# Optimization experiments

Hardware: AMD Instinct MI355X
Metric: run time of the kernel (lower is better)

The kernel has to match this reference:

```python
import jax, jax.numpy as jnp
import numpy as np

B, N, E = 16, 512, 131072
FEAT, EMB, H = 3, 512, 3
K1, K2 = 410, 205  # ceil(0.8*512), ceil(0.5*410) per PyG TopKPooling
NEG_SLOPE, EPS = 0.2, 1e-5


def _gat_conv(x, W, att_s, att_d, bias, src, tgt, valid, num_nodes):
    # PyG GATConv (concat=True): per-edge attention with segment softmax over targets.
    Hh, C = att_s.shape
    xp = (x @ W).reshape(-1, Hh, C)                      # [Nn,H,C]
    a_s = jnp.einsum('nhc,hc->nh', xp, att_s)
    a_d = jnp.einsum('nhc,hc->nh', xp, att_d)
    srcc = jnp.where(valid, src, 0)
    tgtc = jnp.where(valid, tgt, 0)
    e = jax.nn.leaky_relu(a_s[srcc] + a_d[tgtc], NEG_SLOPE)  # [Ee,H]
    seg = jnp.where(valid, tgt, num_nodes)               # invalid edges -> dummy segment
    emax = jax.ops.segment_max(e, seg, num_segments=num_nodes + 1)
    emax = jnp.where(jnp.isfinite(emax), emax, 0.0)
    ex = jnp.exp(e - emax[seg]) * valid[:, None].astype(e.dtype)
    den = jax.ops.segment_sum(ex, seg, num_segments=num_nodes + 1)
    alpha = ex / jnp.maximum(den[seg], 1e-16)            # [Ee,H]
    out = jax.ops.segment_sum(alpha[:, :, None] * xp[srcc], seg,
                              num_segments=num_nodes + 1)[:num_nodes]
    return out.reshape(num_nodes, Hh * C) + bias


def _bn(x, g, b):
    # BatchNorm1d, training-mode batch statistics (biased var), eps=1e-5
    m = x.mean(0)
    v = x.var(0)
    return (x - m) * jax.lax.rsqrt(v + EPS) * g + b


def _topk_pool(x, p, nb, n_per, k):
    # PyG TopKPooling: score = tanh(x.w/||w||), keep top-k per graph, scale by score
    score = jnp.tanh((x @ p) / jnp.linalg.norm(p))       # [nb*n_per]
    top_s, top_i = jax.lax.top_k(score.reshape(nb, n_per), k)
    perm = (top_i + jnp.arange(nb)[:, None] * n_per).reshape(-1)
    x_new = x[perm] * top_s.reshape(-1, 1)
    mapping = jnp.full((nb * n_per,), -1, jnp.int32).at[perm].set(
        jnp.arange(nb * k, dtype=jnp.int32))
    return x_new, mapping


def _pool_cat(x, nb, k):
    # [global_max_pool, global_mean_pool] over equal-size graphs
    xr = x.reshape(nb, k, -1)
    return jnp.concatenate([xr.max(1), xr.mean(1)], axis=1)


def _forward(x, W1, as1, ad1, bc1, Wh1, bh1, g1, be1, p1,
             W2, as2, ad2, bc2, Wh2, bh2, g2, be2, p2,
             Wl1, bl1, Wl2, bl2, edge_index):
    Nn = B * N
    src0, tgt0 = edge_index[0], edge_index[1]
    sl = jnp.arange(Nn, dtype=jnp.int32)                 # GATConv add_self_loops=True
    src1 = jnp.concatenate([src0, sl]); tgt1 = jnp.concatenate([tgt0, sl])
    valid1 = jnp.ones(src1.shape, bool)
    h = _gat_conv(x, W1, as1, ad1, bc1, src1, tgt1, valid1, Nn)
    h = jax.nn.relu(h @ Wh1 + bh1)
    h = _bn(h, g1, be1)
    h, mapping = _topk_pool(h, p1, B, N, K1)
    x1 = _pool_cat(h, B, K1)                             # [B, 2*EMB]
    # relabel edges to pooled node ids; drop edges with removed endpoints via mask
    s2 = mapping[src0]; t2 = mapping[tgt0]
    v2 = (s2 >= 0) & (t2 >= 0)
    sl2 = jnp.arange(B * K1, dtype=jnp.int32)
    src2 = jnp.concatenate([s2, sl2]); tgt2 = jnp.concatenate([t2, sl2])
    valid2 = jnp.concatenate([v2, jnp.ones(sl2.shape, bool)])
    h = _gat_conv(h, W2, as2, ad2, bc2, src2, tgt2, valid2, B * K1)
    h = jax.nn.relu(h @ Wh2 + bh2)
    h = _bn(h, g2, be2)
    h, _ = _topk_pool(h, p2, B, K1, K2)
    x2 = _pool_cat(h, B, K2)
    xg = x1 + x2
    xg = jax.nn.relu(xg @ Wl1 + bl1)                     # dropout p=0.5 disabled (eval)
    return xg @ Wl2 + bl2                                # [B, 256]


def setup_inputs() -> dict:
    key = jax.random.key(0)
    ks = jax.random.split(key, 16)
    x = jax.random.normal(ks[0], (B * N, FEAT), jnp.float32)
    goff = jnp.repeat(jnp.arange(B, dtype=jnp.int32), E // B) * N
    src = jax.random.randint(ks[1], (E,), 0, N, jnp.int32) + goff
    tgt = jax.random.randint(ks[2], (E,), 0, N, jnp.int32) + goff
    edge_index = jnp.stack([src, tgt])
    s = 0.05
    p = {
        'W1': jax.random.normal(ks[3], (FEAT, H * EMB)) * s,
        'as1': jax.random.normal(ks[4], (H, EMB)) * s,
        'ad1': jax.random.normal(ks[5], (H, EMB)) * s,
        'bc1': jnp.zeros((H * EMB,)),
        'Wh1': jax.random.normal(ks[6], (H * EMB, EMB)) * s,
        'bh1': jnp.zeros((EMB,)),
        'g1': jnp.ones((EMB,)), 'be1': jnp.zeros((EMB,)),
        'p1': jax.random.normal(ks[7], (EMB,)) * s,
        'W2': jax.random.normal(ks[8], (EMB, H * EMB)) * s,
        'as2': jax.random.normal(ks[9], (H, EMB)) * s,
        'ad2': jax.random.normal(ks[10], (H, EMB)) * s,
        'bc2': jnp.zeros((H * EMB,)),
        'Wh2': jax.random.normal(ks[11], (H * EMB, EMB)) * s,
        'bh2': jnp.zeros((EMB,)),
        'g2': jnp.ones((EMB,)), 'be2': jnp.zeros((EMB,)),
        'p2': jax.random.normal(ks[12], (EMB,)) * s,
        'Wl1': jax.random.normal(ks[13], (2 * EMB, 512)) * s,
        'bl1': jnp.zeros((512,)),
        'Wl2': jax.random.normal(ks[14], (512, 256)) * s,
        'bl2': jnp.zeros((256,)),
    }
    return {'x': x, 'edge_index': edge_index, **p}


def reference(x, edge_index, W1, as1, ad1, bc1, Wh1, bh1, g1, be1, p1,
              W2, as2, ad2, bc2, Wh2, bh2, g2, be2, p2, Wl1, bl1, Wl2, bl2):
    return _forward(x, W1, as1, ad1, bc1, Wh1, bh1, g1, be1, p1,
                    W2, as2, ad2, bc2, Wh2, bh2, g2, be2, p2,
                    Wl1, bl1, Wl2, bl2, edge_index)
```

## Files before the change

### kernel.cpp

```cpp
#include <hip/hip_runtime.h>
#include <hip/hip_bf16.h>
#include <math.h>

#define E_EDGES 131072
#define NN1 8192
#define NN2 6560
#define NG 16
#define NP1 512
#define KP1 410
#define KP2 205
#define F1 1536
#define EMB 512
#define MAXDEG 256

typedef __hip_bfloat16 bf16;
typedef __attribute__((ext_vector_type(8))) short short8;
typedef __attribute__((ext_vector_type(4))) float f32x4;
typedef __attribute__((ext_vector_type(4))) unsigned short us4;

__device__ inline float wred64(float v){
  #pragma unroll
  for (int o = 32; o; o >>= 1) v += __shfl_down(v, o);
  return v;
}
__device__ inline float b2f_raw(unsigned short u){
  return __uint_as_float((unsigned)u << 16);
}
union BFU { bf16 b; unsigned short u; };
__device__ inline unsigned short f2u(float v){ BFU x; x.b = __float2bfloat16(v); return x.u; }

__device__ __forceinline__ void gld16(const void* g, void* l){
  __builtin_amdgcn_global_load_lds(
      (const __attribute__((address_space(1))) void*)g,
      (__attribute__((address_space(3))) void*)l, 16, 0, 0);
}

__device__ inline void split_store(float v, bf16* __restrict__ ph, bf16* __restrict__ pl){
  bf16 hi = __float2bfloat16(v);
  *ph = hi;
  *pl = __float2bfloat16(v - __bfloat162float(hi));
}

__device__ inline void bn_from_acc(const float* __restrict__ bnacc, int c, float fM,
                                   float& mean, float& inv){
  mean = bnacc[c] / fM;
  float var = fmaxf(bnacc[512+c]/fM - mean*mean, 0.f);
  inv = 1.f / sqrtf(var + 1e-5f);
}

__global__ __launch_bounds__(256) void k_pre(
    const float* __restrict__ W1, const float* __restrict__ as1, const float* __restrict__ ad1,
    const float* __restrict__ Wh1, const float* __restrict__ bc1, const float* __restrict__ bh1,
    const float* __restrict__ W2, const float* __restrict__ as2, const float* __restrict__ ad2,
    const float* __restrict__ Wh2, const float* __restrict__ bc2, const float* __restrict__ bh2,
    const int* __restrict__ src0, const int* __restrict__ tgt0, const float* __restrict__ x,
    float* __restrict__ M1p, float* __restrict__ cvp,
    float* __restrict__ was2, float* __restrict__ wad2,
    float* __restrict__ Zb, int* __restrict__ cnt2, int* __restrict__ map,
    bf16* __restrict__ Th, bf16* __restrict__ Tl,
    float* __restrict__ denp, float* __restrict__ nump){
  int b = blockIdx.x, t = threadIdx.x;
  if (b < 24){
    int h = b / 8, rem = b % 8, jh = rem >> 2, kc = rem & 3;
    int j = jh*256 + t, c0 = kc*128;
    __shared__ float w1s[3][128];
    for (int i = t; i < 384; i += 256)
      w1s[i>>7][i&127] = W1[(i>>7)*1536 + h*512 + c0 + (i&127)];
    __syncthreads();
    const float* whc = Wh1 + (size_t)(h*512 + c0)*512 + j;
    float a0=0.f, a1=0.f, a2=0.f;
    #pragma unroll 8
    for (int c = 0; c < 128; c++){
      float v = whc[(size_t)c*512];
      a0 += w1s[0][c]*v; a1 += w1s[1][c]*v; a2 += w1s[2][c]*v;
    }
    float* dst = M1p + (size_t)kc*4608;
    dst[(h*3+0)*512 + j] = a0;
    dst[(h*3+1)*512 + j] = a1;
    dst[(h*3+2)*512 + j] = a2;
  } else if (b < 56){
    int b2 = b - 24;
    int which = b2 >> 4, rem = b2 & 15, jh = rem >> 3, kc = rem & 7;
    const float* bc = which ? bc2 : bc1;
    const float* Wh = which ? Wh2 : Wh1;
    const float* bh = which ? bh2 : bh1;
    int j = jh*256 + t, i0 = kc*192;
    float acc = (kc == 0) ? bh[j] : 0.f;
    #pragma unroll 8
    for (int i = 0; i < 192; i++)
      acc += bc[i0+i] * Wh[(size_t)(i0+i)*512 + j];
    cvp[(size_t)(which*8 + kc)*512 + j] = acc;
  } else if (b < 152){
    int b3 = b - 56;
    int y = b3 >> 4, et = b3 & 15;
    int kind = y / 3, h = y % 3;
    int w = t >> 6, lane = t & 63;
    const float* att = kind ? ad2 : as2;
    float a[8];
    #pragma unroll
    for (int u = 0; u < 8; u++) a[u] = att[h*512 + lane*8 + u];
    for (int r = w; r < 32; r += 4){
      int e = et*32 + r;
      const float4* row = (const float4*)(W2 + (size_t)e*1536 + h*512) + lane*2;
      float4 v0 = row[0], v1 = row[1];
      float d = v0.x*a[0]+v0.y*a[1]+v0.z*a[2]+v0.w*a[3]
              + v1.x*a[4]+v1.y*a[5]+v1.z*a[6]+v1.w*a[7];
      d = wred64(d);
      if (lane == 0) (kind ? wad2 : was2)[h*512 + e] = d;
    }
  } else if (b < 218){
    int i = (b - 152)*256 + t;
    if (i < 2048){ Zb[i] = 0.f; }
    else if (i < 2048 + NN2){ cnt2[i - 2048] = 1; }
    else if (i < 2048 + NN2 + NN1){ map[i - 2048 - NN2] = -1; }
  } else if (b < 474){
    __shared__ float sww[18];
    __shared__ float lden[1536];
    __shared__ float lnum[4608];
    int wv_ = t >> 6, lane = t & 63;
    for (int combo = wv_*5; combo < wv_*5+5 && combo < 18; combo++){
      int kind = combo/9, rr = combo%9, h = rr/3, f = rr%3;
      const float* att = kind ? ad1 : as1;
      float s = 0.f;
      #pragma unroll
      for (int c = lane; c < 512; c += 64) s += W1[f*1536 + h*512 + c] * att[h*512 + c];
      s = wred64(s);
      if (lane == 0) sww[combo] = s;
    }
    for (int i = t; i < 1536; i += 256) lden[i] = 0.f;
    for (int i = t; i < 4608; i += 256) lnum[i] = 0.f;
    __syncthreads();
    int eb = b - 218;
    int g = eb >> 4, ch = eb & 15;
    int base = g*8192;
    int it0 = ch*544;
    for (int k = t; k < 544; k += 256){
      int it = it0 + k;
      int s, tl;
      if (it < 8192){ s = src0[base+it]; tl = tgt0[base+it] & 511; }
      else { tl = it - 8192; s = g*512 + tl; }
      float xs0 = x[s*3], xs1 = x[s*3+1], xs2 = x[s*3+2];
      int tg = g*512 + tl;
      float xt0 = x[tg*3], xt1 = x[tg*3+1], xt2 = x[tg*3+2];
      #pragma unroll
      for (int h = 0; h < 3; h++){
        float v = xs0*sww[h*3]+xs1*sww[h*3+1]+xs2*sww[h*3+2]
                + xt0*sww[9+h*3]+xt1*sww[9+h*3+1]+xt2*sww[9+h*3+2];
        v = v > 0.f ? v : 0.2f*v;
        float pe = expf(v);
        atomicAdd(&lden[tl*3 + h], pe);
        atomicAdd(&lnum[tl*9 + h*3 + 0], pe * xs0);
        atomicAdd(&lnum[tl*9 + h*3 + 1], pe * xs1);
        atomicAdd(&lnum[tl*9 + h*3 + 2], pe * xs2);
      }
    }
    __syncthreads();
    for (int i = t; i < 4608; i += 256) nump[(size_t)eb*4608 + i] = lnum[i];
    for (int i = t; i < 1536; i += 256) denp[(size_t)eb*1536 + i] = lden[i];
  } else {
    int bb = b - 474;
    int z = bb % 3; int rr = bb / 3; int by = rr >> 3, bx = rr & 7;
    const float* A = W2 + (size_t)z*512;
    const float* B = Wh2 + (size_t)z*512*512;
    __shared__ __align__(16) short sAh[4096], sAl[4096], sBh[4096], sBl[4096];
    int w = t >> 6, lane = t & 63;
    int l16 = lane & 15, q = lane >> 4;
    int bm = by*64, bn = bx*64;
    int am  = t >> 2, akw = (t & 3)*16;
    int bnl = t & 63, bkq = (t >> 6)*16;
    f32x4 acc[4];
    #pragma unroll
    for (int nf = 0; nf < 4; nf++) acc[nf] = (f32x4){0.f,0.f,0.f,0.f};
    float va[16], vb[16];
    #define GS_LOAD(K0) do { \
      _Pragma("unroll") for (int u = 0; u < 4; u++){ \
        float4 v4 = *(const float4*)(A + (size_t)(bm+am)*1536 + (K0) + akw + u*4); \
        va[u*4]=v4.x; va[u*4+1]=v4.y; va[u*4+2]=v4.z; va[u*4+3]=v4.w; } \
      _Pragma("unroll") for (int u = 0; u < 16; u++) \
        vb[u] = B[(size_t)((K0) + bkq + u)*512 + bn + bnl]; \
    } while(0)
    GS_LOAD(0);
    for (int it = 0; it < 8; it++){
      #pragma unroll
      for (int hh = 0; hh < 2; hh++){
        short8 ah_, al_, bh_, bl_;
        #pragma unroll
        for (int jj = 0; jj < 8; jj++){
          float v = va[hh*8+jj];
          unsigned short hu = f2u(v);
          ah_[jj] = (short)hu; al_[jj] = (short)f2u(v - b2f_raw(hu));
          v = vb[hh*8+jj];
          hu = f2u(v);
          bh_[jj] = (short)hu; bl_[jj] = (short)f2u(v - b2f_raw(hu));
        }
        int aoff = am*64  + ((((akw>>3) + hh) ^ (am  & 7)) << 3);
        *(short8*)(sAh + aoff) = ah_;
        *(short8*)(sAl + aoff) = al_;
        int boff = bnl*64 + ((((bkq>>3) + hh) ^ (bnl & 7)) << 3);
        *(short8*)(sBh + boff) = bh_;
        *(short8*)(sBl + boff) = bl_;
      }
      __syncthreads();
      if (it < 7) GS_LOAD((it+1)*64);
      #pragma unroll
      for (int ks = 0; ks < 2; ks++){
        int gc = ks*4 + q;
        int ar = w*16 + l16;
        int ao = ar*64 + ((gc ^ (ar & 7)) << 3);
        short8 afh = *(const short8*)(sAh + ao);
        short8 afl = *(const short8*)(sAl + ao);
        #pragma unroll
        for (int nf = 0; nf < 4; nf++){
          int br = nf*16 + l16;
          int bo = br*64 + ((gc ^ (br & 7)) << 3);
          short8 bfh = *(const short8*)(sBh + bo);
          short8 bfl = *(const short8*)(sBl + bo);
          acc[nf] = __builtin_amdgcn_mfma_f32_16x16x32_bf16(afh, bfh, acc[nf], 0, 0, 0);
          acc[nf] = __builtin_amdgcn_mfma_f32_16x16x32_bf16(afh, bfl, acc[nf], 0, 0, 0);
          acc[nf] = __builtin_amdgcn_mfma_f32_16x16x32_bf16(afl, bfh, acc[nf], 0, 0, 0);
        }
      }
      __syncthreads();
    }
    #undef GS_LOAD
    int m0 = bm + w*16 + q*4;
    #pragma unroll
    for (int nf = 0; nf < 4; nf++){
      int n = bn + nf*16 + l16;
      size_t base = (size_t)n*1536 + (size_t)z*512 + m0;
      #pragma unroll
      for (int e = 0; e < 4; e++)
        split_store(acc[nf][e], &Th[base+e], &Tl[base+e]);
    }
  }
}

__global__ __launch_bounds__(256) void k_h1(
    const float* __restrict__ nump, const float* __restrict__ denp,
    const float* __restrict__ M1p, const float* __restrict__ cvp1, bf16* __restrict__ hout,
    float* __restrict__ bnacc1){
  __shared__ float sM[9*512];
  __shared__ float sC[512];
  __shared__ float sA[32*9];
  int t = threadIdx.x; int n0 = blockIdx.x*32;
  for (int i = t; i < 9*512; i += 256)
    sM[i] = M1p[i] + M1p[4608 + i] + M1p[2*4608 + i] + M1p[3*4608 + i];
  for (int i = t; i < 512; i += 256){
    float s = 0.f;
    #pragma unroll
    for (int kc = 0; kc < 8; kc++) s += cvp1[kc*512 + i];
    sC[i] = s;
  }
  for (int i = t; i < 288; i += 256){
    int node = i / 9, q = i % 9, hh = q / 3;
    int gn = n0 + node;
    int g = gn >> 9, nl = gn & 511;
    float ns = 0.f, ds = 0.f;
    #pragma unroll 4
    for (int ch = 0; ch < 16; ch++){
      ns += nump[(size_t)(g*16 + ch)*4608 + nl*9 + q];
      ds += denp[(size_t)(g*16 + ch)*1536 + nl*3 + hh];
    }
    sA[i] = ns / fmaxf(ds, 1e-16f);
  }
  __syncthreads();
  float c0v = sC[t], c1v = sC[t+256];
  float ls0=0.f, lq0=0.f, ls1=0.f, lq1=0.f;
  #pragma unroll 4
  for (int i = 0; i < 32; i++){
    float a0 = c0v, a1 = c1v;
    #pragma unroll
    for (int q = 0; q < 9; q++){
      float av = sA[i*9+q];
      a0 += av * sM[q*512 + t];
      a1 += av * sM[q*512 + t + 256];
    }
    a0 = fmaxf(a0, 0.f); a1 = fmaxf(a1, 0.f);
    hout[(size_t)(n0+i)*512 + t]       = __float2bfloat16(a0);
    hout[(size_t)(n0+i)*512 + t + 256] = __float2bfloat16(a1);
    ls0 += a0; lq0 += a0*a0; ls1 += a1; lq1 += a1*a1;
  }
  atomicAdd(&bnacc1[t],           ls0);
  atomicAdd(&bnacc1[t+256],       ls1);
  atomicAdd(&bnacc1[512 + t],     lq0);
  atomicAdd(&bnacc1[512 + t+256], lq1);
}

__global__ __launch_bounds__(512) void k_scoresort(
    const bf16* __restrict__ h, const float* __restrict__ bnacc, int M,
    const float* __restrict__ g_, const float* __restrict__ be, const float* __restrict__ p,
    int n_per, int K, int* __restrict__ map,
    int* __restrict__ topi, float* __restrict__ tops, float* __restrict__ cat){
  int g = blockIdx.x, t = threadIdx.x;
  __shared__ float w[512];
  __shared__ float redb[8], redp[8];
  __shared__ float sk[512];
  __shared__ int si[512];
  float fM = (float)M;
  float mean, inv; bn_from_acc(bnacc, t, fM, mean, inv);
  float gc = g_[t], pc = p[t], bec = be[t];
  float ig = inv * gc;
  w[t] = ig * pc;
  float bt = (bec - mean * ig) * pc;
  float b_ = wred64(bt);
  float pp = wred64(pc * pc);
  int lane = t & 63, wv = t >> 6;
  if (lane == 0){ redb[wv] = b_; redp[wv] = pp; }
  __syncthreads();
  float B0 = 0.f, pn2 = 0.f;
  #pragma unroll
  for (int u = 0; u < 8; u++){ B0 += redb[u]; pn2 += redp[u]; }
  float pn = sqrtf(pn2);
  float score = -INFINITY; int idx = 0x7fffffff;
  if (t < n_per){
    const unsigned short* hr = (const unsigned short*)h + (size_t)(g*n_per + t)*EMB;
    float dot = 0.f;
    #pragma unroll 4
    for (int c = 0; c < 512; c += 8){
      us4 v0 = *(const us4*)(hr + c);
      us4 v1 = *(const us4*)(hr + c + 4);
      dot += b2f_raw(v0.x)*w[c]   + b2f_raw(v0.y)*w[c+1]
           + b2f_raw(v0.z)*w[c+2] + b2f_raw(v0.w)*w[c+3]
           + b2f_raw(v1.x)*w[c+4] + b2f_raw(v1.y)*w[c+5]
           + b2f_raw(v1.z)*w[c+6] + b2f_raw(v1.w)*w[c+7];
    }
    score = tanhf((dot + B0) / pn);
    idx = t;
  }
  sk[t] = score; si[t] = idx;
  __syncthreads();
  for (int k = 2; k <= 512; k <<= 1){
    for (int j = k >> 1; j > 0; j >>= 1){
      int l = t ^ j;
      if (l > t){
        float ki = sk[t], kl = sk[l]; int ii = si[t], il = si[l];
        bool before_l = (kl > ki) || (kl == ki && il < ii);
        bool up = ((t & k) == 0);
        if (up == before_l){ sk[t]=kl; sk[l]=ki; si[t]=il; si[l]=ii; }
      }
      __syncthreads();
    }
  }
  if (cat == nullptr){
    if (t < K){
      if (map) map[g*n_per + si[t]] = g*K + t;
      topi[g*K + t] = si[t];
      tops[g*K + t] = sk[t];
    }
  } else {
    const unsigned short* hp = (const unsigned short*)h;
    float mx = -INFINITY, sm = 0.f;
    for (int r = 0; r < K; r++){
      float v = (b2f_raw(hp[(size_t)(g*n_per + si[r])*EMB + t]) - mean) * ig + bec;
      v *= sk[r];
      mx = fmaxf(mx, v); sm += v;
    }
    cat[g*1024 + t] = mx;
    cat[g*1024 + 512 + t] = sm / (float)K;
  }
}

__global__ __launch_bounds__(256) void k_gather_c2(
    const bf16* __restrict__ h, const float* __restrict__ bnacc, int M,
    const float* __restrict__ gm, const float* __restrict__ be,
    const int* __restrict__ topi, const float* __restrict__ tops,
    bf16* __restrict__ xn, int n_per, int K,
    const float* __restrict__ was2, const float* __restrict__ wad2,
    float* __restrict__ aso, float* __restrict__ ado,
    const int* __restrict__ src0, const int* __restrict__ tgt0,
    const int* __restrict__ map, int* __restrict__ cnt2, int nblk_g){
  int row = blockIdx.x, t = threadIdx.x;
  if (row >= nblk_g){
    int i = (row - nblk_g)*256 + t;
    if (i < E_EDGES){
      int s = map[src0[i]], tg = map[tgt0[i]];
      if (s >= 0 && tg >= 0) atomicAdd(&cnt2[tg], 1);
    }
    return;
  }
  int gr = row / K, i = row - gr*K;
  int sidx = topi[gr*K + i];
  float s = tops[gr*K + i];
  const bf16* src = h + ((size_t)(gr*n_per + sidx))*EMB;
  bf16* dst = xn + (size_t)row*EMB;
  int c0 = t, c1 = t + 256;
  float fM = (float)M;
  float mean0, inv0, mean1, inv1;
  bn_from_acc(bnacc, c0, fM, mean0, inv0);
  bn_from_acc(bnacc, c1, fM, mean1, inv1);
  float v0 = ((__bfloat162float(src[c0]) - mean0) * inv0 * gm[c0] + be[c0]) * s;
  float v1 = ((__bfloat162float(src[c1]) - mean1) * inv1 * gm[c1] + be[c1]) * s;
  dst[c0] = __float2bfloat16(v0);
  dst[c1] = __float2bfloat16(v1);
  {
    float a[6];
    #pragma unroll
    for (int hh = 0; hh < 3; hh++){
      a[hh]   = v0*was2[hh*512 + c0] + v1*was2[hh*512 + c1];
      a[3+hh] = v0*wad2[hh*512 + c0] + v1*wad2[hh*512 + c1];
    }
    __shared__ float red[6][4];
    int lane = t & 63, wv = t >> 6;
    #pragma unroll
    for (int q = 0; q < 6; q++){ float v = wred64(a[q]); if (lane==0) red[q][wv]=v; }
    __syncthreads();
    if (t < 6){
      float sm = red[t][0]+red[t][1]+red[t][2]+red[t][3];
      if (t < 3) aso[row*3+t] = sm; else ado[row*3+(t-3)] = sm;
    }
  }
}

__device__ inline void scan_body(const int* __restrict__ counts, int* __restrict__ off,
                                 int* __restrict__ cur, int n, int* __restrict__ sh){
  int t = threadIdx.x;
  int chunk = (n + 1023) >> 10;
  int b = t * chunk; int e = b + chunk; if (e > n) e = n;
  int s = 0;
  for (int i = b; i < e; i++) s += counts[i];
  sh[t] = s; __syncthreads();
  for (int o = 1; o < 1024; o <<= 1){
    int v = (t >= o) ? sh[t-o] : 0;
    __syncthreads();
    sh[t] += v;
    __syncthreads();
  }
  int run = (t > 0) ? sh[t-1] : 0;
  for (int i = b; i < e; i++){ int c = counts[i]; off[i] = run; cur[i] = run; run += c; }
  if (t == 1023) off[n] = sh[1023];
}
__global__ void k_fill2(const int* __restrict__ src0, const int* __restrict__ tgt0,
                        const int* __restrict__ map, int* __restrict__ cur,
                        int* __restrict__ esrc, int E, int nn){
  int i = blockIdx.x*blockDim.x + threadIdx.x;
  if (i >= E + nn) return;
  int s, tg;
  if (i < E){
    s = map[src0[i]]; tg = map[tgt0[i]];
    if (s < 0 || tg < 0) return;
  } else { s = i - E; tg = s; }
  int pos = atomicAdd(&cur[tg], 1);
  esrc[pos] = s;
}

__global__ __launch_bounds__(1024) void k_poolA_scan(const bf16* __restrict__ xn,
    float* __restrict__ cat, int K,
    const int* __restrict__ cnt2, int* __restrict__ off2, int* __restrict__ cur2){
  __shared__ int shi[1024];
  __shared__ float smax[8][128];
  __shared__ float ssum[8][128];
  int b = blockIdx.x, t = threadIdx.x;
  if (b == 64){ scan_body(cnt2, off2, cur2, NN2, shi); return; }
  int g = b >> 2, cb = b & 3;
  int c = t & 127, rg = t >> 7;
  int col = cb*128 + c;
  const unsigned short* p = (const unsigned short*)xn + (size_t)g*K*EMB + col;
  float mx = -INFINITY, sm = 0.f;
  for (int r = rg; r < K; r += 8){
    float v = b2f_raw(p[(size_t)r*EMB]);
    mx = fmaxf(mx, v); sm += v;
  }
  smax[rg][c] = mx; ssum[rg][c] = sm;
  __syncthreads();
  if (rg == 0){
    #pragma unroll
    for (int u = 1; u < 8; u++){ mx = fmaxf(mx, smax[u][c]); sm += ssum[u][c]; }
    cat[g*1024 + col] = mx;
    cat[g*1024 + 512 + col] = sm / (float)K;
  }
}

__global__ __launch_bounds__(256) void k_agg2(
    const bf16* __restrict__ xn, const float* __restrict__ aso, const float* __restrict__ ado,
    const int* __restrict__ off, const int* __restrict__ esrc,
    bf16* __restrict__ oh){
  int n = blockIdx.x, t = threadIdx.x;
  __shared__ int srcs[MAXDEG];
  __shared__ float al[MAXDEG*3];
  __shared__ float mh[3], dh[3];
  int s0 = off[n]; int deg = off[n+1] - s0; if (deg > MAXDEG) deg = MAXDEG;
  for (int e = t; e < deg; e += 256) srcs[e] = esrc[s0 + e];
  __syncthreads();
  float ad0 = ado[n*3+0], ad1 = ado[n*3+1], ad2 = ado[n*3+2];
  for (int e = t; e < deg; e += 256){
    int s = srcs[e];
    float v0 = aso[s*3+0] + ad0, v1 = aso[s*3+1] + ad1, v2 = aso[s*3+2] + ad2;
    al[e*3+0] = v0 > 0.f ? v0 : 0.2f*v0;
    al[e*3+1] = v1 > 0.f ? v1 : 0.2f*v1;
    al[e*3+2] = v2 > 0.f ? v2 : 0.2f*v2;
  }
  __syncthreads();
  if (t < 3){
    float m = -INFINITY;
    for (int e = 0; e < deg; e++) m = fmaxf(m, al[e*3+t]);
    float d = 0.f;
    for (int e = 0; e < deg; e++) d += expf(al[e*3+t] - m);
    mh[t] = m; dh[t] = 1.f / fmaxf(d, 1e-16f);
  }
  __syncthreads();
  for (int e = t; e < deg; e += 256){
    al[e*3+0] = expf(al[e*3+0]-mh[0])*dh[0];
    al[e*3+1] = expf(al[e*3+1]-mh[1])*dh[1];
    al[e*3+2] = expf(al[e*3+2]-mh[2])*dh[2];
  }
  __syncthreads();
  float acc[2][3] = {};
  for (int e = 0; e < deg; e++){
    int s = srcs[e];
    float a0 = al[e*3], a1 = al[e*3+1], a2 = al[e*3+2];
    #pragma unroll
    for (int k = 0; k < 2; k++){
      float v = __bfloat162float(xn[(size_t)s*512 + t + k*256]);
      acc[k][0] += a0*v; acc[k][1] += a1*v; acc[k][2] += a2*v;
    }
  }
  #pragma unroll
  for (int k = 0; k < 2; k++){
    int c = t + k*256;
    #pragma unroll
    for (int h = 0; h < 3; h++)
      oh[(size_t)n*1536 + h*512 + c] = __float2bfloat16(acc[k][h]);
  }
}

__global__ __launch_bounds__(256, 2) void k_gemm_mfma(
    const bf16* __restrict__ Ah,
    const bf16* __restrict__ Bh, const bf16* __restrict__ Bl,
    const float* __restrict__ bias, bf16* __restrict__ C,
    float* __restrict__ bnacc,
    int M, int N, int K, int Mtiles){
  int xcd = (int)blockIdx.x & 7;
  int ii  = (int)blockIdx.x >> 3;
  int bni = ii & 7;
  int bmi = xcd + 8*(ii >> 3);
  if (bmi >= Mtiles) return;
  __shared__ __align__(16) unsigned short lds[2][16384];
  int t = threadIdx.x, w = t >> 6, lane = t & 63;
  int q = lane >> 4, l16 = lane & 15;
  int bm = bmi * 128, bn = bni * 64;

  int lr = lane >> 3, lc = lane & 7;
  int kg = ((lc ^ lr) & 7) * 8;
  int ro = w*8 + lr;
  int m0 = bm + ro, m1 = bm + 32 + ro, m2 = bm + 64 + ro, m3 = bm + 96 + ro;
  if (m0 >= M) m0 = M-1;  if (m1 >= M) m1 = M-1;
  if (m2 >= M) m2 = M-1;  if (m3 >= M) m3 = M-1;
  int n0 = bn + ro, n1 = bn + 32 + ro;
  const bf16* ptr[8];
  ptr[0] = Ah + (size_t)m0*K + kg;
  ptr[1] = Ah + (size_t)m1*K + kg;
  ptr[2] = Ah + (size_t)m2*K + kg;
  ptr[3] = Ah + (size_t)m3*K + kg;
  ptr[4] = Bh + (size_t)n0*K + kg;
  ptr[5] = Bh + (size_t)n1*K + kg;
  ptr[6] = Bl + (size_t)n0*K + kg;
  ptr[7] = Bl + (size_t)n1*K + kg;
  const int dof[8] = {0, 2048, 4096, 6144, 8192, 10240, 12288, 14336};

  int wm = (w >> 1) * 64, wn = (w & 1) * 32;
  f32x4 acc[4][2];
  #pragma unroll
  for (int i = 0; i < 4; i++)
    #pragma unroll
    for (int j = 0; j < 2; j++)
      acc[i][j] = (f32x4){0.f, 0.f, 0.f, 0.f};

  #pragma unroll
  for (int u = 0; u < 8; u++){
    gld16(ptr[u], &lds[0][dof[u] + w*512]);
    ptr[u] += 64;
  }

  int nit = K >> 6;
  for (int it = 0; it < nit; it++){
    __syncthreads();
    int cur = it & 1;
    if (it + 1 < nit){
      int nxt = cur ^ 1;
      #pragma unroll
      for (int u = 0; u < 8; u++){
        gld16(ptr[u], &lds[nxt][dof[u] + w*512]);
        ptr[u] += 64;
      }
    }
    const unsigned short* L = lds[cur];
    #pragma unroll
    for (int ks = 0; ks < 2; ks++){
      short8 ah[4], bh2[2], bl2[2];
      int gc = ks*4 + q;
      #pragma unroll
      for (int i = 0; i < 4; i++){
        int r = wm + i*16 + l16;
        ah[i] = *(const short8*)(L + r*64 + ((gc ^ (r & 7)) << 3));
      }
      #pragma unroll
      for (int j = 0; j < 2; j++){
        int r = wn + j*16 + l16;
        int so = ((gc ^ (r & 7)) << 3);
        bh2[j] = *(const short8*)(L + 8192  + r*64 + so);
        bl2[j] = *(const short8*)(L + 12288 + r*64 + so);
      }
      #pragma unroll
      for (int i = 0; i < 4; i++)
        #pragma unroll
        for (int j = 0; j < 2; j++){
          acc[i][j] = __builtin_amdgcn_mfma_f32_16x16x32_bf16(ah[i], bh2[j], acc[i][j], 0, 0, 0);
          acc[i][j] = __builtin_amdgcn_mfma_f32_16x16x32_bf16(ah[i], bl2[j], acc[i][j], 0, 0, 0);
        }
    }
  }

  __syncthreads();
  float* cs = (float*)&lds[0][0];
  float* cq = cs + 128;
  int slot = w >> 1;
  #pragma unroll
  for (int j = 0; j < 2; j++){
    int c_local = wn + j*16 + l16;
    int c = bn + c_local;
    float bv = 0.f;
    if (bias){
      #pragma unroll
      for (int kc = 0; kc < 8; kc++) bv += bias[kc*512 + c];
    }
    float ls = 0.f, lq = 0.f;
    #pragma unroll
    for (int i = 0; i < 4; i++){
      int rb = bm + wm + i*16 + q*4;
      #pragma unroll
      for (int e = 0; e < 4; e++){
        int r = rb + e;
        if (r < M){
          float v = fmaxf(acc[i][j][e] + bv, 0.f);
          C[(size_t)r*N + c] = __float2bfloat16(v);
          ls += v; lq += v*v;
        }
      }
    }
    ls += __shfl_xor(ls, 16); ls += __shfl_xor(ls, 32);
    lq += __shfl_xor(lq, 16); lq += __shfl_xor(lq, 32);
    if (q == 0){ cs[slot*64 + c_local] = ls; cq[slot*64 + c_local] = lq; }
  }
  __syncthreads();
  if (t < 64){
    atomicAdd(&bnacc[bn + t],        cs[t] + cs[64 + t]);
    atomicAdd(&bnacc[512 + bn + t],  cq[t] + cq[64 + t]);
  }
}

__global__ __launch_bounds__(256) void k_head1p(const float* __restrict__ c1,
    const float* __restrict__ c2, const float* __restrict__ Wl1,
    float* __restrict__ t1p){
  __shared__ float wl[128][64];
  __shared__ float xgs[16][128];
  int b = blockIdx.x, t = threadIdx.x;
  int jt = b >> 3, kc = b & 7;
  int j0 = jt*64, k0 = kc*128;
  for (int i = t; i < 8192; i += 256){
    int k = i >> 6, j = i & 63;
    wl[k][j] = Wl1[(size_t)(k0 + k)*512 + j0 + j];
  }
  for (int i = t; i < 2048; i += 256){
    int g = i >> 7, k = i & 127;
    int idx = g*1024 + k0 + k;
    xgs[g][k] = c1[idx] + c2[idx];
  }
  __syncthreads();
  #pragma unroll
  for (int u = 0; u < 4; u++){
    int p = t + u*256;
    int g = p >> 6, j = p & 63;
    float acc = 0.f;
    #pragma unroll 8
    for (int k = 0; k < 128; k++)
      acc += xgs[g][k] * wl[k][j];
    t1p[(size_t)(kc*16 + g)*512 + j0 + j] = acc;
  }
}
__global__ __launch_bounds__(512) void k_head2p(const float* __restrict__ t1p,
    const float* __restrict__ bl1, const float* __restrict__ Wl2,
    const float* __restrict__ bl2, float* __restrict__ out){
  __shared__ float t1s[512];
  __shared__ float part[2][256];
  int g = blockIdx.x, t = threadIdx.x;
  float acc = bl1[t];
  #pragma unroll
  for (int kc = 0; kc < 8; kc++)
    acc += t1p[(size_t)(kc*16 + g)*512 + t];
  t1s[t] = fmaxf(acc, 0.f);
  __syncthreads();
  int c = t & 255, half = t >> 8;
  float a = 0.f;
  #pragma unroll 8
  for (int k = half*256; k < half*256 + 256; k++)
    a += t1s[k] * Wl2[(size_t)k*256 + c];
  part[half][c] = a;
  __syncthreads();
  if (half == 0)
    out[g*256 + c] = part[0][c] + part[1][c] + bl2[c];
}

extern "C" void kernel_launch(void* const* d_in, const int* in_sizes, int n_in,
                              void* d_out, int out_size, void* d_ws, size_t ws_size,
                              hipStream_t stream){
  const float* x   = (const float*)d_in[0];
  const int*   ei  = (const int*)d_in[1];
  const float* W1  = (const float*)d_in[2];
  const float* as1 = (const float*)d_in[3];
  const float* ad1 = (const float*)d_in[4];
  const float* bc1 = (const float*)d_in[5];
  const float* Wh1 = (const float*)d_in[6];
  const float* bh1 = (const float*)d_in[7];
  const float* g1  = (const float*)d_in[8];
  const float* be1 = (const float*)d_in[9];
  const float* p1  = (const float*)d_in[10];
  const float* W2  = (const float*)d_in[11];
  const float* as2 = (const float*)d_in[12];
  const float* ad2 = (const float*)d_in[13];
  const float* bc2 = (const float*)d_in[14];
  const float* Wh2 = (const float*)d_in[15];
  const float* bh2 = (const float*)d_in[16];
  const float* g2  = (const float*)d_in[17];
  const float* be2 = (const float*)d_in[18];
  const float* p2  = (const float*)d_in[19];
  const float* Wl1 = (const float*)d_in[20];
  const float* bl1 = (const float*)d_in[21];
  const float* Wl2 = (const float*)d_in[22];
  const float* bl2 = (const float*)d_in[23];
  float* out = (float*)d_out;

  const int* src0 = ei;
  const int* tgt0 = ei + E_EDGES;

  bf16* Cc      = (bf16*)d_ws;
  bf16* xn1     = Cc + (size_t)NN1*EMB;
  bf16* aggx2h  = xn1 + (size_t)NN2*EMB;
  bf16* M2Th    = aggx2h + (size_t)NN2*F1;
  bf16* M2Tl    = M2Th + (size_t)EMB*F1;
  float* holeA  = (float*)(M2Tl + (size_t)EMB*F1);
  float* t1p    = holeA;
  float* bnacc1 = holeA + 122880;
  float* bnacc  = bnacc1 + 1024;
  float* M1p    = bnacc + 1024;
  float* cvp    = M1p + 4*4608;
  float* was2   = cvp + 16*512;
  float* wad2   = was2 + 3*512;
  float* hole16 = wad2 + 3*512;
  float* aso2   = hole16 + 32;
  float* ado2   = aso2 + (size_t)NN2*3;
  float* tops   = ado2 + (size_t)NN2*3;
  float* cat1   = tops + NG*KP1;
  float* cat2   = cat1 + NG*1024;
  int* topi     = (int*)(cat2 + NG*1024);
  int* map      = topi + NG*KP1;
  int* cnt2     = map + NN1;
  int* off2     = cnt2 + NN2;
  int* cur2     = off2 + NN2 + 8;
  int* esrc2    = cur2 + NN2;
  float* nump   = (float*)(esrc2 + 137700);
  float* denp   = nump + (size_t)256*4608;
  float* cvp2   = cvp + 8*512;

  k_pre<<<666,256,0,stream>>>(W1,as1,ad1,Wh1,bc1,bh1, W2,as2,ad2,Wh2,bc2,bh2,
                              src0,tgt0,x,
                              M1p,cvp,was2,wad2,
                              bnacc1,cnt2,map,M2Th,M2Tl, denp,nump);
  k_h1<<<NN1/32,256,0,stream>>>(nump,denp,M1p,cvp,Cc,bnacc1);
  k_scoresort<<<NG,512,0,stream>>>(Cc,bnacc1,NN1,g1,be1,p1,NP1,KP1,map,topi,tops,
                                   (float*)nullptr);
  k_gather_c2<<<NG*KP1+512,256,0,stream>>>(Cc,bnacc1,NN1,g1,be1,topi,tops,xn1,NP1,KP1,
      was2,wad2,aso2,ado2, src0,tgt0,map,cnt2,NG*KP1);
  k_poolA_scan<<<65,1024,0,stream>>>(xn1,cat1,KP1, cnt2,off2,cur2);
  k_fill2<<<(E_EDGES+NN2+255)/256,256,0,stream>>>(src0,tgt0,map,cur2,esrc2,E_EDGES,NN2);
  k_agg2<<<NN2,256,0,stream>>>(xn1,aso2,ado2,off2,esrc2,aggx2h);
  k_gemm_mfma<<<448,256,0,stream>>>(aggx2h,M2Th,M2Tl,cvp2,Cc,bnacc,NN2,EMB,F1,52);
  k_scoresort<<<NG,512,0,stream>>>(Cc,bnacc,NN2,g2,be2,p2,KP1,KP2,(int*)nullptr,
                                   (int*)nullptr,(float*)nullptr,cat2);
  k_head1p<<<64,256,0,stream>>>(cat1,cat2,Wl1,t1p);
  k_head2p<<<NG,512,0,stream>>>(t1p,bl1,Wl2,bl2,out);
}
```

Baseline: 310.0 us.

## Split score computation from per-graph sort into a wide row-parallel kernel

The TopK score dot products used to run inside a 16-block sort kernel, one thread per row scanning 512 features. They now run in a separate kernel with one wavefront per row, spread over hundreds of blocks, with coalesced loads and a shuffle reduction. The sort and pooling kernels then read the scores from a workspace buffer. This adds two extra launches and a small global round trip in exchange for much higher parallelism on the score phase.

```diff
diff --git a/kernel.cpp b/kernel.cpp
--- a/kernel.cpp
+++ b/kernel.cpp
@@ -286,48 +286,58 @@
   atomicAdd(&bnacc1[512 + t+256], lq1);
 }
 
-__global__ __launch_bounds__(512) void k_scoresort(
+__global__ __launch_bounds__(256) void k_score(
     const bf16* __restrict__ h, const float* __restrict__ bnacc, int M,
     const float* __restrict__ g_, const float* __restrict__ be, const float* __restrict__ p,
-    int n_per, int K, int* __restrict__ map,
-    int* __restrict__ topi, float* __restrict__ tops, float* __restrict__ cat){
+    float* __restrict__ score, int NR){
+  __shared__ float w[512];
+  __shared__ float rb[4], rp[4];
+  int t = threadIdx.x;
+  int lane = t & 63, wv = t >> 6;
+  float fM = (float)M;
+  float bt = 0.f, pp = 0.f;
+  #pragma unroll
+  for (int k = 0; k < 2; k++){
+    int c = t + k*256;
+    float mean, inv; bn_from_acc(bnacc, c, fM, mean, inv);
+    float gc = g_[c], pc = p[c];
+    float ig = inv * gc;
+    w[c] = ig * pc;
+    bt += (be[c] - mean * ig) * pc;
+    pp += pc * pc;
+  }
+  bt = wred64(bt); pp = wred64(pp);
+  if (lane == 0){ rb[wv] = bt; rp[wv] = pp; }
+  __syncthreads();
+  float B0 = rb[0]+rb[1]+rb[2]+rb[3];
+  float pn = sqrtf(rp[0]+rp[1]+rp[2]+rp[3]);
+  float wl[8];
+  #pragma unroll
+  for (int u = 0; u < 8; u++) wl[u] = w[lane*8 + u];
+  int rbase = blockIdx.x*32 + wv*8;
+  for (int rr = 0; rr < 8; rr++){
+    int r = rbase + rr;
+    if (r >= NR) break;
+    const unsigned short* hr = (const unsigned short*)h + (size_t)r*EMB + lane*8;
+    us4 v0 = *(const us4*)(hr);
+    us4 v1 = *(const us4*)(hr + 4);
+    float dot = b2f_raw(v0.x)*wl[0] + b2f_raw(v0.y)*wl[1]
+              + b2f_raw(v0.z)*wl[2] + b2f_raw(v0.w)*wl[3]
+              + b2f_raw(v1.x)*wl[4] + b2f_raw(v1.y)*wl[5]
+              + b2f_raw(v1.z)*wl[6] + b2f_raw(v1.w)*wl[7];
+    dot = wred64(dot);
+    if (lane == 0) score[r] = tanhf((dot + B0) / pn);
+  }
+}
+
+__global__ __launch_bounds__(512) void k_sort1(
+    const float* __restrict__ score, int n_per, int K,
+    int* __restrict__ map, int* __restrict__ topi, float* __restrict__ tops){
   int g = blockIdx.x, t = threadIdx.x;
-  __shared__ float w[512];
-  __shared__ float redb[8], redp[8];
   __shared__ float sk[512];
   __shared__ int si[512];
-  float fM = (float)M;
-  float mean, inv; bn_from_acc(bnacc, t, fM, mean, inv);
-  float gc = g_[t], pc = p[t], bec = be[t];
-  float ig = inv * gc;
-  w[t] = ig * pc;
-  float bt = (bec - mean * ig) * pc;
-  float b_ = wred64(bt);
-  float pp = wred64(pc * pc);
-  int lane = t & 63, wv = t >> 6;
-  if (lane == 0){ redb[wv] = b_; redp[wv] = pp; }
-  __syncthreads();
-  float B0 = 0.f, pn2 = 0.f;
-  #pragma unroll
-  for (int u = 0; u < 8; u++){ B0 += redb[u]; pn2 += redp[u]; }
-  float pn = sqrtf(pn2);
-  float score = -INFINITY; int idx = 0x7fffffff;
-  if (t < n_per){
-    const unsigned short* hr = (const unsigned short*)h + (size_t)(g*n_per + t)*EMB;
-    float dot = 0.f;
-    #pragma unroll 4
-    for (int c = 0; c < 512; c += 8){
-      us4 v0 = *(const us4*)(hr + c);
-      us4 v1 = *(const us4*)(hr + c + 4);
-      dot += b2f_raw(v0.x)*w[c]   + b2f_raw(v0.y)*w[c+1]
-           + b2f_raw(v0.z)*w[c+2] + b2f_raw(v0.w)*w[c+3]
-           + b2f_raw(v1.x)*w[c+4] + b2f_raw(v1.y)*w[c+5]
-           + b2f_raw(v1.z)*w[c+6] + b2f_raw(v1.w)*w[c+7];
-    }
-    score = tanhf((dot + B0) / pn);
-    idx = t;
-  }
-  sk[t] = score; si[t] = idx;
+  if (t < n_per){ sk[t] = score[g*n_per + t]; si[t] = t; }
+  else { sk[t] = -INFINITY; si[t] = 0x7fffffff; }
   __syncthreads();
   for (int k = 2; k <= 512; k <<= 1){
     for (int j = k >> 1; j > 0; j >>= 1){
@@ -341,23 +351,48 @@
       __syncthreads();
     }
   }
-  if (cat == nullptr){
-    if (t < K){
-      if (map) map[g*n_per + si[t]] = g*K + t;
-      topi[g*K + t] = si[t];
-      tops[g*K + t] = sk[t];
-    }
-  } else {
-    const unsigned short* hp = (const unsigned short*)h;
-    float mx = -INFINITY, sm = 0.f;
-    for (int r = 0; r < K; r++){
-      float v = (b2f_raw(hp[(size_t)(g*n_per + si[r])*EMB + t]) - mean) * ig + bec;
-      v *= sk[r];
-      mx = fmaxf(mx, v); sm += v;
-    }
-    cat[g*1024 + t] = mx;
-    cat[g*1024 + 512 + t] = sm / (float)K;
-  }
+  if (t < K){
+    map[g*n_per + si[t]] = g*K + t;
+    topi[g*K + t] = si[t];
+    tops[g*K + t] = sk[t];
+  }
+}
+
+__global__ __launch_bounds__(512) void k_sortpool2(
+    const bf16* __restrict__ h, const float* __restrict__ score,
+    const float* __restrict__ bnacc, int M,
+    const float* __restrict__ g_, const float* __restrict__ be,
+    int n_per, int K, float* __restrict__ cat){
+  int g = blockIdx.x, t = threadIdx.x;
+  __shared__ float sk[512];
+  __shared__ int si[512];
+  if (t < n_per){ sk[t] = score[g*n_per + t]; si[t] = t; }
+  else { sk[t] = -INFINITY; si[t] = 0x7fffffff; }
+  __syncthreads();
+  for (int k = 2; k <= 512; k <<= 1){
+    for (int j = k >> 1; j > 0; j >>= 1){
+      int l = t ^ j;
+      if (l > t){
+        float ki = sk[t], kl = sk[l]; int ii = si[t], il = si[l];
+        bool before_l = (kl > ki) || (kl == ki && il < ii);
+        bool up = ((t & k) == 0);
+        if (up == before_l){ sk[t]=kl; sk[l]=ki; si[t]=il; si[l]=ii; }
+      }
+      __syncthreads();
+    }
+  }
+  float fM = (float)M;
+  float mean, inv; bn_from_acc(bnacc, t, fM, mean, inv);
+  float ig = inv * g_[t], bec = be[t];
+  const unsigned short* hp = (const unsigned short*)h;
+  float mx = -INFINITY, sm = 0.f;
+  for (int r = 0; r < K; r++){
+    float v = (b2f_raw(hp[(size_t)(g*n_per + si[r])*EMB + t]) - mean) * ig + bec;
+    v *= sk[r];
+    mx = fmaxf(mx, v); sm += v;
+  }
+  cat[g*1024 + t] = mx;
+  cat[g*1024 + 512 + t] = sm / (float)K;
 }
 
 __global__ __launch_bounds__(256) void k_gather_c2(
@@ -739,6 +774,7 @@
   bf16* M2Tl    = M2Th + (size_t)EMB*F1;
   float* holeA  = (float*)(M2Tl + (size_t)EMB*F1);
   float* t1p    = holeA;
+  float* score  = holeA + 65536;
   float* bnacc1 = holeA + 122880;
   float* bnacc  = bnacc1 + 1024;
   float* M1p    = bnacc + 1024;
@@ -766,16 +802,16 @@
                               M1p,cvp,was2,wad2,
                               bnacc1,cnt2,map,M2Th,M2Tl, denp,nump);
   k_h1<<<NN1/32,256,0,stream>>>(nump,denp,M1p,cvp,Cc,bnacc1);
-  k_scoresort<<<NG,512,0,stream>>>(Cc,bnacc1,NN1,g1,be1,p1,NP1,KP1,map,topi,tops,
-                                   (float*)nullptr);
+  k_score<<<NN1/32,256,0,stream>>>(Cc,bnacc1,NN1,g1,be1,p1,score,NN1);
+  k_sort1<<<NG,512,0,stream>>>(score,NP1,KP1,map,topi,tops);
   k_gather_c2<<<NG*KP1+512,256,0,stream>>>(Cc,bnacc1,NN1,g1,be1,topi,tops,xn1,NP1,KP1,
       was2,wad2,aso2,ado2, src0,tgt0,map,cnt2,NG*KP1);
   k_poolA_scan<<<65,1024,0,stream>>>(xn1,cat1,KP1, cnt2,off2,cur2);
   k_fill2<<<(E_EDGES+NN2+255)/256,256,0,stream>>>(src0,tgt0,map,cur2,esrc2,E_EDGES,NN2);
   k_agg2<<<NN2,256,0,stream>>>(xn1,aso2,ado2,off2,esrc2,aggx2h);
   k_gemm_mfma<<<448,256,0,stream>>>(aggx2h,M2Th,M2Tl,cvp2,Cc,bnacc,NN2,EMB,F1,52);
-  k_scoresort<<<NG,512,0,stream>>>(Cc,bnacc,NN2,g2,be2,p2,KP1,KP2,(int*)nullptr,
-                                   (int*)nullptr,(float*)nullptr,cat2);
+  k_score<<<(NN2+31)/32,256,0,stream>>>(Cc,bnacc,NN2,g2,be2,p2,score,NN2);
+  k_sortpool2<<<NG,512,0,stream>>>(Cc,score,bnacc,NN2,g2,be2,KP1,KP2,cat2);
   k_head1p<<<64,256,0,stream>>>(cat1,cat2,Wl1,t1p);
   k_head2p<<<NG,512,0,stream>>>(t1p,bl1,Wl2,bl2,out);
 }
```

Result: no change. 308.1 us (median of 2 runs) (-0.6%).
